# Kernel optimization log

Hardware: AMD Instinct MI355X
Metric: run time of the kernel (lower is better)

The kernel has to match this reference:

```python
import jax, jax.numpy as jnp
import numpy as np

N_NODES = 50000
N_EDGES = 800000
D_FEAT = 64
UNITS = 64


def setup_inputs() -> dict:
    key = jax.random.key(0)
    k1, k2, k3, k4, k5 = jax.random.split(key, 5)
    embeddings = jax.random.normal(k1, (N_NODES, D_FEAT), dtype=jnp.float32)
    edge_src = jax.random.randint(k2, (N_EDGES,), 0, N_NODES, dtype=jnp.int32)
    edge_dst = jax.random.randint(k3, (N_EDGES,), 0, N_NODES, dtype=jnp.int32)
    # normalized-adjacency-like positive weights
    edge_w = jax.random.uniform(k4, (N_EDGES,), dtype=jnp.float32)
    # keras 'truncated_normal' initializer default stddev=0.05 (approx w/ normal)
    kernel = jax.random.normal(k5, (D_FEAT, UNITS), dtype=jnp.float32) * 0.05
    return {"embeddings": embeddings, "edge_src": edge_src,
            "edge_dst": edge_dst, "edge_w": edge_w, "kernel": kernel}


def reference(embeddings, edge_src, edge_dst, edge_w, kernel):
    # SpMM: agg[i] = sum_{e: dst(e)=i} w_e * embeddings[src(e)]
    msgs = embeddings[edge_src] * edge_w[:, None]            # [E, D]
    agg = jax.ops.segment_sum(msgs, edge_dst,
                              num_segments=embeddings.shape[0])  # [N, D]
    # dense GEMM + relu (use_bias=False)
    return jax.nn.relu(agg @ kernel)                          # [N, units]
```

## Files before the change

### kernel.cpp

```cpp
#include <hip/hip_runtime.h>
#include <hip/hip_bf16.h>

#define D    64
#define CH   4096
#define BKT  32
#define PASS 1024
#define SU   2048

__global__ __launch_bounds__(256) void gemm_part(
    const float* __restrict__ emb,
    const float* __restrict__ W,
    __hip_bfloat16* __restrict__ Zb,
    const int*   __restrict__ dst,
    int*         __restrict__ histG,
    int N, int E, int NB, int NC, int gemmTiles)
{
    __shared__ int smem[4096];

    if ((int)blockIdx.x >= gemmTiles) {
        const int c   = (int)blockIdx.x - gemmTiles;
        const int t   = threadIdx.x;
        const int e0  = c * CH;
        const int cnt = min(CH, E - e0);
        for (int b = t; b < NB; b += 256) smem[b] = 0;
        __syncthreads();
        const int4* d4p = reinterpret_cast<const int4*>(dst + e0);
#pragma unroll
        for (int i = 0; i < 4; ++i) {
            int g = i * 256 + t;
            if (g * 4 < cnt) {
                int4 d4 = d4p[g];
                atomicAdd(&smem[d4.x >> 5], 1);
                atomicAdd(&smem[d4.y >> 5], 1);
                atomicAdd(&smem[d4.z >> 5], 1);
                atomicAdd(&smem[d4.w >> 5], 1);
            }
        }
        __syncthreads();
        for (int b = t; b < NB; b += 256)
            histG[(size_t)b * NC + c] = smem[b];
        return;
    }

    const int lane = threadIdx.x & 63;
    const int wave = threadIdx.x >> 6;

    float wcol[D];
#pragma unroll
    for (int k = 0; k < D; ++k) wcol[k] = W[k * D + lane];

    float* At = (float*)smem;
    const int row0 = blockIdx.x * 64;

    for (int i = threadIdx.x; i < 1024; i += 256) {
        int r = i >> 4, gr = row0 + r;
        float4 v = (gr < N)
            ? reinterpret_cast<const float4*>(emb)[(size_t)gr * 16 + (i & 15)]
            : float4{0.f, 0.f, 0.f, 0.f};
        reinterpret_cast<float4*>(At)[i] = v;
    }
    __syncthreads();

    for (int rr = 0; rr < 16; ++rr) {
        int r = wave * 16 + rr, gr = row0 + r;
        if (gr >= N) break;
        const float4* arow = reinterpret_cast<const float4*>(At + r * D);
        float acc = 0.f;
#pragma unroll
        for (int k4 = 0; k4 < 16; ++k4) {
            float4 a = arow[k4];
            acc = fmaf(a.x, wcol[4 * k4 + 0], acc);
            acc = fmaf(a.y, wcol[4 * k4 + 1], acc);
            acc = fmaf(a.z, wcol[4 * k4 + 2], acc);
            acc = fmaf(a.w, wcol[4 * k4 + 3], acc);
        }
        Zb[(size_t)gr * D + lane] = __float2bfloat16(acc);
    }
}

__global__ __launch_bounds__(256) void scan_hist(
    const int* __restrict__ histG, int* __restrict__ offsets,
    int* __restrict__ partials, int M)
{
    __shared__ int sh[256];
    const int t    = threadIdx.x;
    const int base = blockIdx.x * SU + t * 8;

    int v[8], ps[8];
#pragma unroll
    for (int k = 0; k < 8; ++k) {
        int m = base + k;
        v[k] = (m < M) ? histG[m] : 0;
    }
    int s = 0;
#pragma unroll
    for (int k = 0; k < 8; ++k) { ps[k] = s; s += v[k]; }
    sh[t] = s;
    __syncthreads();
    for (int off = 1; off < 256; off <<= 1) {
        int x = (t >= off) ? sh[t - off] : 0;
        __syncthreads();
        sh[t] += x;
        __syncthreads();
    }
    const int excl = sh[t] - s;
#pragma unroll
    for (int k = 0; k < 8; ++k)
        offsets[base + k] = excl + ps[k];
    if (t == 255) partials[blockIdx.x] = sh[255];
}

__global__ __launch_bounds__(256) void scan_partials_k(
    int* __restrict__ partials, int units)
{
    __shared__ int sh[256];
    const int t    = threadIdx.x;
    const int orig = (t < units) ? partials[t] : 0;
    sh[t] = orig;
    __syncthreads();
    for (int off = 1; off < 256; off <<= 1) {
        int x = (t >= off) ? sh[t - off] : 0;
        __syncthreads();
        sh[t] += x;
        __syncthreads();
    }
    if (t < units) partials[t] = sh[t] - orig;
}

__global__ __launch_bounds__(256) void scatter_bkt(
    const int*   __restrict__ src,
    const int*   __restrict__ dst,
    const float* __restrict__ w,
    const int*   __restrict__ offsets,
    const int*   __restrict__ partials,
    int2*        __restrict__ csr,
    int E, int NB, int NC)
{
    __shared__ int2 rec[CH];
    __shared__ int  lcnt[1568];
    __shared__ int  sh[256];

    const int t   = threadIdx.x;
    const int c   = blockIdx.x;
    const int e0  = c * CH;
    const int cnt = min(CH, E - e0);

    for (int b = t; b < NB; b += 256) lcnt[b] = 0;
    __syncthreads();

    int2 myrec[16]; int mypos[16];
    const int4*   s4p = reinterpret_cast<const int4*>(src + e0);
    const int4*   d4p = reinterpret_cast<const int4*>(dst + e0);
    const float4* w4p = reinterpret_cast<const float4*>(w + e0);
#pragma unroll
    for (int i = 0; i < 4; ++i) {
        int g = i * 256 + t;
        if (g * 4 < cnt) {
            int4   s4 = s4p[g];
            int4   d4 = d4p[g];
            float4 w4 = w4p[g];
            int b0 = d4.x >> 5, b1 = d4.y >> 5, b2 = d4.z >> 5, b3 = d4.w >> 5;
            myrec[4*i+0] = make_int2(s4.x | ((d4.x & 31) << 16) | (b0 << 21), __float_as_int(w4.x));
            myrec[4*i+1] = make_int2(s4.y | ((d4.y & 31) << 16) | (b1 << 21), __float_as_int(w4.y));
            myrec[4*i+2] = make_int2(s4.z | ((d4.z & 31) << 16) | (b2 << 21), __float_as_int(w4.z));
            myrec[4*i+3] = make_int2(s4.w | ((d4.w & 31) << 16) | (b3 << 21), __float_as_int(w4.w));
            mypos[4*i+0] = atomicAdd(&lcnt[b0], 1);
            mypos[4*i+1] = atomicAdd(&lcnt[b1], 1);
            mypos[4*i+2] = atomicAdd(&lcnt[b2], 1);
            mypos[4*i+3] = atomicAdd(&lcnt[b3], 1);
        } else {
#pragma unroll
            for (int k = 0; k < 4; ++k) mypos[4*i+k] = -1;
        }
    }
    __syncthreads();

    int hv[7], ps[7];
    const int hbase = t * 7;
#pragma unroll
    for (int k = 0; k < 7; ++k) {
        int b = hbase + k;
        hv[k] = (b < NB) ? lcnt[b] : 0;
    }
    int s = 0;
#pragma unroll
    for (int k = 0; k < 7; ++k) { ps[k] = s; s += hv[k]; }
    sh[t] = s;
    __syncthreads();
    for (int off = 1; off < 256; off <<= 1) {
        int x = (t >= off) ? sh[t - off] : 0;
        __syncthreads();
        sh[t] += x;
        __syncthreads();
    }
    const int hexcl = sh[t] - s;
    __syncthreads();
#pragma unroll
    for (int k = 0; k < 7; ++k) {
        int b = hbase + k;
        if (b < NB) lcnt[b] = hexcl + ps[k];
    }
    __syncthreads();

#pragma unroll
    for (int k = 0; k < 16; ++k) {
        if (mypos[k] >= 0)
            rec[lcnt[(unsigned)myrec[k].x >> 21] + mypos[k]] = myrec[k];
    }
    __syncthreads();

#pragma unroll
    for (int k = 0; k < 7; ++k) {
        int b = hbase + k;
        if (b < NB) {
            int m = b * NC + c;
            lcnt[b] = offsets[m] + partials[m >> 11] - lcnt[b];
        }
    }
    __syncthreads();

    for (int j = t; j < cnt; j += 256) {
        int2 rj = rec[j];
        csr[j + lcnt[(unsigned)rj.x >> 21]] = rj;
    }
}

__global__ __launch_bounds__(256) void aggregate(
    const __hip_bfloat16* __restrict__ Zb,
    const int2* __restrict__ csr,
    const int*  __restrict__ offsets,
    const int*  __restrict__ partials,
    float*      __restrict__ out,
    int N, int NB, int NC)
{
    __shared__ int2 srec[PASS];
    __shared__ int  hist[BKT];
    __shared__ int  nbase[BKT + 1];

    const int t = threadIdx.x;
    const int b = blockIdx.x;

    const int m0 = b * NC, m1 = m0 + NC;
    const int bStart = offsets[m0] + partials[m0 >> 11];
    const int bEnd   = offsets[m1] + partials[m1 >> 11];

    const int wv = t >> 6, lane = t & 63, slot = lane >> 3, q = lane & 7;
    const int4* Zq = reinterpret_cast<const int4*>(Zb);

    float4 alo[8], ahi[8];
#pragma unroll
    for (int r = 0; r < 8; ++r) { alo[r] = float4{0,0,0,0}; ahi[r] = float4{0,0,0,0}; }

#define FMA8(LO, HI, WW, ZZ)                                                     \
    do {                                                                         \
        (LO).x = fmaf((WW), __uint_as_float((unsigned)(ZZ).x << 16),        (LO).x); \
        (LO).y = fmaf((WW), __uint_as_float((unsigned)(ZZ).x & 0xFFFF0000u),(LO).y); \
        (LO).z = fmaf((WW), __uint_as_float((unsigned)(ZZ).y << 16),        (LO).z); \
        (LO).w = fmaf((WW), __uint_as_float((unsigned)(ZZ).y & 0xFFFF0000u),(LO).w); \
        (HI).x = fmaf((WW), __uint_as_float((unsigned)(ZZ).z << 16),        (HI).x); \
        (HI).y = fmaf((WW), __uint_as_float((unsigned)(ZZ).z & 0xFFFF0000u),(HI).y); \
        (HI).z = fmaf((WW), __uint_as_float((unsigned)(ZZ).w << 16),        (HI).z); \
        (HI).w = fmaf((WW), __uint_as_float((unsigned)(ZZ).w & 0xFFFF0000u),(HI).w); \
    } while (0)

    for (int cur = bStart; cur < bEnd; cur += PASS) {
        const int cnt = min(PASS, bEnd - cur);
        if (t < BKT) hist[t] = 0;
        __syncthreads();

        int2 myrec[4]; int mypos[4];
#pragma unroll
        for (int k = 0; k < 4; ++k) {
            int j = k * 256 + t;
            if (j < cnt) {
                int2 r2 = csr[cur + j];
                myrec[k] = r2;
                mypos[k] = atomicAdd(&hist[(r2.x >> 16) & (BKT - 1)], 1);
            } else mypos[k] = -1;
        }
        __syncthreads();

        if (t < BKT) {
            int v = hist[t], x = v;
            for (int off = 1; off < BKT; off <<= 1) {
                int y = __shfl_up(x, off, 64);
                if (t >= off) x += y;
            }
            nbase[t] = x - v;
            if (t == BKT - 1) nbase[BKT] = x;
        }
        __syncthreads();

#pragma unroll
        for (int k = 0; k < 4; ++k) {
            if (mypos[k] >= 0)
                srec[nbase[(myrec[k].x >> 16) & (BKT - 1)] + mypos[k]] = myrec[k];
        }
        __syncthreads();

        for (int r = 0; r < 8; ++r) {
            const int nl = wv * 8 + r;
            const int jb = nbase[nl] + slot;
            const int je = nbase[nl + 1];
            const int j1 = jb + 8, j2 = jb + 16;
            int2 e0 = make_int2(0, 0), e1 = make_int2(0, 0), e2 = make_int2(0, 0);
            if (jb < je) e0 = srec[jb];
            if (j1 < je) e1 = srec[j1];
            if (j2 < je) e2 = srec[j2];
            int4 z0 = make_int4(0,0,0,0), z1 = make_int4(0,0,0,0), z2 = make_int4(0,0,0,0);
            if (jb < je) z0 = Zq[(size_t)(e0.x & 0xFFFF) * 8 + q];
            if (j1 < je) z1 = Zq[(size_t)(e1.x & 0xFFFF) * 8 + q];
            if (j2 < je) z2 = Zq[(size_t)(e2.x & 0xFFFF) * 8 + q];
            FMA8(alo[r], ahi[r], __int_as_float(e0.y), z0);
            FMA8(alo[r], ahi[r], __int_as_float(e1.y), z1);
            FMA8(alo[r], ahi[r], __int_as_float(e2.y), z2);
            for (int j = j2 + 8; j < je; j += 8) {
                int2 e = srec[j];
                int4 zz = Zq[(size_t)(e.x & 0xFFFF) * 8 + q];
                FMA8(alo[r], ahi[r], __int_as_float(e.y), zz);
            }
        }
        __syncthreads();
    }

    const int node0 = b * BKT + wv * 8;
#pragma unroll
    for (int r = 0; r < 8; ++r) {
        float4 lo = alo[r], hi = ahi[r];
#pragma unroll
        for (int off = 32; off >= 8; off >>= 1) {
            lo.x += __shfl_down(lo.x, off, 64);
            lo.y += __shfl_down(lo.y, off, 64);
            lo.z += __shfl_down(lo.z, off, 64);
            lo.w += __shfl_down(lo.w, off, 64);
            hi.x += __shfl_down(hi.x, off, 64);
            hi.y += __shfl_down(hi.y, off, 64);
            hi.z += __shfl_down(hi.z, off, 64);
            hi.w += __shfl_down(hi.w, off, 64);
        }
        int node = node0 + r;
        if (lane < 8 && node < N) {
            float4 o0, o1;
            o0.x = fmaxf(lo.x, 0.f); o0.y = fmaxf(lo.y, 0.f);
            o0.z = fmaxf(lo.z, 0.f); o0.w = fmaxf(lo.w, 0.f);
            o1.x = fmaxf(hi.x, 0.f); o1.y = fmaxf(hi.y, 0.f);
            o1.z = fmaxf(hi.z, 0.f); o1.w = fmaxf(hi.w, 0.f);
            float4* orow = reinterpret_cast<float4*>(out) + (size_t)node * 16 + lane * 2;
            orow[0] = o0;
            orow[1] = o1;
        }
    }
#undef FMA8
}

extern "C" void kernel_launch(void* const* d_in, const int* in_sizes, int n_in,
                              void* d_out, int out_size, void* d_ws, size_t ws_size,
                              hipStream_t stream)
{
    const float* emb  = (const float*)d_in[0];
    const int*   esrc = (const int*)  d_in[1];
    const int*   edst = (const int*)  d_in[2];
    const float* ew   = (const float*)d_in[3];
    const float* W    = (const float*)d_in[4];
    float*       out  = (float*)d_out;

    const int N = in_sizes[0] / D;
    const int E = in_sizes[1];

    const int NB    = (N + BKT - 1) / BKT;
    const int NC    = (E + CH - 1) / CH;
    const int M     = NB * NC;
    const int units = (M + SU - 1) / SU;
    const int Mpad  = units * SU;
    const int gemmTiles = (N + 63) / 64;

    char* p = (char*)d_ws;
    __hip_bfloat16* Zb = (__hip_bfloat16*)p;  p += (size_t)N * D * 2;
    int*  histG    = (int*)p;                 p += (size_t)Mpad * 4;
    int*  offsets  = (int*)p;                 p += (size_t)Mpad * 4;
    int*  partials = (int*)p;                 p += 256 * 4;
    int2* csr      = (int2*)p;

    gemm_part<<<gemmTiles + NC, 256, 0, stream>>>(
        emb, W, Zb, edst, histG, N, E, NB, NC, gemmTiles);

    scan_hist<<<units, 256, 0, stream>>>(histG, offsets, partials, M);

    scan_partials_k<<<1, 256, 0, stream>>>(partials, units);

    scatter_bkt<<<NC, 256, 0, stream>>>(
        esrc, edst, ew, offsets, partials, csr, E, NB, NC);

    aggregate<<<NB, 256, 0, stream>>>(
        Zb, csr, offsets, partials, out, N, NB, NC);
}
```

Before: 137.3 us.

## Split Z feature columns into two halves and aggregate each in a separate pass

The GEMM now writes Z as two column-half planes (N x 32 bf16 each), and aggregation runs twice, once per half, with 16 edge slots of 4 lanes each instead of 8 slots of 8 lanes. The aim is to halve the gather working set per pass (3.2 MB per half) so it stays cache-resident, and to raise edge-level parallelism per row. The cost is reading the CSR records and scanning buckets twice, plus an extra kernel launch.

```diff
diff --git a/kernel.cpp b/kernel.cpp
--- a/kernel.cpp
+++ b/kernel.cpp
@@ -61,6 +61,10 @@
     }
     __syncthreads();
 
+    const int half = lane >> 5;
+    const int fo   = lane & 31;
+    __hip_bfloat16* Zh = Zb + (size_t)half * N * 32;
+
     for (int rr = 0; rr < 16; ++rr) {
         int r = wave * 16 + rr, gr = row0 + r;
         if (gr >= N) break;
@@ -74,7 +78,7 @@
             acc = fmaf(a.z, wcol[4 * k4 + 2], acc);
             acc = fmaf(a.w, wcol[4 * k4 + 3], acc);
         }
-        Zb[(size_t)gr * D + lane] = __float2bfloat16(acc);
+        Zh[(size_t)gr * 32 + fo] = __float2bfloat16(acc);
     }
 }
 
@@ -225,13 +229,13 @@
     }
 }
 
-__global__ __launch_bounds__(256) void aggregate(
-    const __hip_bfloat16* __restrict__ Zb,
+__global__ __launch_bounds__(256) void aggregate_half(
+    const __hip_bfloat16* __restrict__ Zh,
     const int2* __restrict__ csr,
     const int*  __restrict__ offsets,
     const int*  __restrict__ partials,
     float*      __restrict__ out,
-    int N, int NB, int NC)
+    int N, int NB, int NC, int h)
 {
     __shared__ int2 srec[PASS];
     __shared__ int  hist[BKT];
@@ -244,8 +248,10 @@
     const int bStart = offsets[m0] + partials[m0 >> 11];
     const int bEnd   = offsets[m1] + partials[m1 >> 11];
 
-    const int wv = t >> 6, lane = t & 63, slot = lane >> 3, q = lane & 7;
-    const int4* Zq = reinterpret_cast<const int4*>(Zb);
+    const int wv = t >> 6, lane = t & 63;
+    const int slot = lane >> 2;
+    const int q    = lane & 3;
+    const int4* Zq = reinterpret_cast<const int4*>(Zh);
 
     float4 alo[8], ahi[8];
 #pragma unroll
@@ -302,21 +308,18 @@
             const int nl = wv * 8 + r;
             const int jb = nbase[nl] + slot;
             const int je = nbase[nl + 1];
-            const int j1 = jb + 8, j2 = jb + 16;
-            int2 e0 = make_int2(0, 0), e1 = make_int2(0, 0), e2 = make_int2(0, 0);
+            const int j1 = jb + 16;
+            int2 e0 = make_int2(0, 0), e1 = make_int2(0, 0);
             if (jb < je) e0 = srec[jb];
             if (j1 < je) e1 = srec[j1];
-            if (j2 < je) e2 = srec[j2];
-            int4 z0 = make_int4(0,0,0,0), z1 = make_int4(0,0,0,0), z2 = make_int4(0,0,0,0);
-            if (jb < je) z0 = Zq[(size_t)(e0.x & 0xFFFF) * 8 + q];
-            if (j1 < je) z1 = Zq[(size_t)(e1.x & 0xFFFF) * 8 + q];
-            if (j2 < je) z2 = Zq[(size_t)(e2.x & 0xFFFF) * 8 + q];
+            int4 z0 = make_int4(0,0,0,0), z1 = make_int4(0,0,0,0);
+            if (jb < je) z0 = Zq[(size_t)(e0.x & 0xFFFF) * 4 + q];
+            if (j1 < je) z1 = Zq[(size_t)(e1.x & 0xFFFF) * 4 + q];
             FMA8(alo[r], ahi[r], __int_as_float(e0.y), z0);
             FMA8(alo[r], ahi[r], __int_as_float(e1.y), z1);
-            FMA8(alo[r], ahi[r], __int_as_float(e2.y), z2);
-            for (int j = j2 + 8; j < je; j += 8) {
+            for (int j = j1 + 16; j < je; j += 16) {
                 int2 e = srec[j];
-                int4 zz = Zq[(size_t)(e.x & 0xFFFF) * 8 + q];
+                int4 zz = Zq[(size_t)(e.x & 0xFFFF) * 4 + q];
                 FMA8(alo[r], ahi[r], __int_as_float(e.y), zz);
             }
         }
@@ -328,7 +331,7 @@
     for (int r = 0; r < 8; ++r) {
         float4 lo = alo[r], hi = ahi[r];
 #pragma unroll
-        for (int off = 32; off >= 8; off >>= 1) {
+        for (int off = 32; off >= 4; off >>= 1) {
             lo.x += __shfl_down(lo.x, off, 64);
             lo.y += __shfl_down(lo.y, off, 64);
             lo.z += __shfl_down(lo.z, off, 64);
@@ -339,13 +342,14 @@
             hi.w += __shfl_down(hi.w, off, 64);
         }
         int node = node0 + r;
-        if (lane < 8 && node < N) {
+        if (lane < 4 && node < N) {
             float4 o0, o1;
             o0.x = fmaxf(lo.x, 0.f); o0.y = fmaxf(lo.y, 0.f);
             o0.z = fmaxf(lo.z, 0.f); o0.w = fmaxf(lo.w, 0.f);
             o1.x = fmaxf(hi.x, 0.f); o1.y = fmaxf(hi.y, 0.f);
             o1.z = fmaxf(hi.z, 0.f); o1.w = fmaxf(hi.w, 0.f);
-            float4* orow = reinterpret_cast<float4*>(out) + (size_t)node * 16 + lane * 2;
+            float4* orow = reinterpret_cast<float4*>(out)
+                         + (size_t)node * 16 + h * 8 + lane * 2;
             orow[0] = o0;
             orow[1] = o1;
         }
@@ -391,6 +395,9 @@
     scatter_bkt<<<NC, 256, 0, stream>>>(
         esrc, edst, ew, offsets, partials, csr, E, NB, NC);
 
-    aggregate<<<NB, 256, 0, stream>>>(
-        Zb, csr, offsets, partials, out, N, NB, NC);
-}
+    aggregate_half<<<NB, 256, 0, stream>>>(
+        Zb, csr, offsets, partials, out, N, NB, NC, 0);
+
+    aggregate_half<<<NB, 256, 0, stream>>>(
+        Zb + (size_t)N * 32, csr, offsets, partials, out, N, NB, NC, 1);
+}
```

Result: slower. 168.1 us (+22.4%).
